# Performance work log

Hardware: AMD Instinct MI355X
Metric: run time of the kernel (lower is better)

The kernel has to match this reference:

```python
import jax, jax.numpy as jnp
import numpy as np

TAU = 2.0        # MultiStepLIFNode tau
ALPHA = 4.0      # sigmoid surrogate-gradient sharpness (spikingjelly default)
BN_EPS = 1e-5

@jax.custom_vjp
def heaviside(x):
    return (x >= 0.0).astype(x.dtype)

def _h_fwd(x):
    return (x >= 0.0).astype(x.dtype), x

def _h_bwd(res, g):
    s = jax.nn.sigmoid(ALPHA * res)
    return (g * ALPHA * s * (1.0 - s),)

heaviside.defvjp(_h_fwd, _h_bwd)

def lif(x_seq, v_threshold=1.0):
    """Multi-step LIF, hard reset to 0, decay_input, detach_reset. x_seq: [T, ...]"""
    def step(v, x):
        v = v + (x - v) / TAU
        spike = heaviside(v - v_threshold)
        v = v * (1.0 - jax.lax.stop_gradient(spike))
        return v, spike
    _, spikes = jax.lax.scan(step, jnp.zeros_like(x_seq[0]), x_seq)
    return spikes

def conv1x1_bn(x, w, gamma, beta, mean, var, bias=None):
    # x: [T,B,C,H,W]; 1x1 conv == channel matmul; BN in eval mode (affine fold)
    y = jnp.einsum('tbchw,oc->tbohw', x, w)
    if bias is not None:
        y = y + bias[None, None, :, None, None]
    inv = gamma / jnp.sqrt(var + BN_EPS)
    return y * inv[None, None, :, None, None] + (beta - mean * inv)[None, None, :, None, None]

def setup_inputs() -> dict:
    key = jax.random.key(0)
    T, B, C, H, W = 4, 16, 512, 32, 32
    ks = jax.random.split(key, 18)
    def w(k):
        return jax.random.normal(k, (C, C), jnp.float32) * (1.0 / np.sqrt(C))
    def vec_n(k):
        return jax.random.normal(k, (C,), jnp.float32) * 0.1
    def vec_p(k):
        return jax.random.uniform(k, (C,), jnp.float32, 0.5, 1.5)
    return {
        'x': jax.random.normal(ks[0], (T, B, C, H, W), jnp.float32),
        'q_w': w(ks[1]), 'q_gamma': vec_p(ks[2]), 'q_beta': vec_n(ks[3]),
        'q_mean': vec_n(ks[4]), 'q_var': vec_p(ks[5]),
        'k_w': w(ks[6]), 'k_gamma': vec_p(ks[7]), 'k_beta': vec_n(ks[8]),
        'k_mean': vec_n(ks[9]), 'k_var': vec_p(ks[10]),
        'proj_w': w(ks[11]), 'proj_b': vec_n(ks[12]), 'proj_gamma': vec_p(ks[13]),
        'proj_beta': vec_n(ks[14]), 'proj_mean': vec_n(ks[15]), 'proj_var': vec_p(ks[16]),
        'num_heads': 8,
    }

def reference(x, q_w, q_gamma, q_beta, q_mean, q_var,
              k_w, k_gamma, k_beta, k_mean, k_var,
              proj_w, proj_b, proj_gamma, proj_beta, proj_mean, proj_var,
              num_heads):
    T, B, C, H, W = x.shape
    hd = C // num_heads
    # Q / K branches: conv1x1 -> BN -> LIF spikes
    q = lif(conv1x1_bn(x, q_w, q_gamma, q_beta, q_mean, q_var))          # [T,B,C,H,W]
    k = lif(conv1x1_bn(x, k_w, k_gamma, k_beta, k_mean, k_var))          # [T,B,C,H,W]
    # sum over head-channel dim (keepdim), spike-gate at threshold 0.5
    q = q.reshape(T, B, num_heads, hd, H, W).sum(axis=3, keepdims=True)  # [T,B,nh,1,H,W]
    attn = lif(q, v_threshold=0.5)                                       # [T,B,nh,1,H,W]
    # elementwise gated attention (broadcast over head channels)
    y = (attn * k.reshape(T, B, num_heads, hd, H, W)).reshape(T, B, C, H, W)
    # projection: conv1x1(+bias) -> BN -> LIF
    y = lif(conv1x1_bn(y, proj_w, proj_gamma, proj_beta, proj_mean, proj_var, bias=proj_b))
    return y
```

## Files before the change

kernel.cpp:

```cpp
#include <hip/hip_runtime.h>
#include <cstdint>
#include <math.h>

#define TT 4
#define BB 16
#define CCH 512
#define HWD 1024
#define NHH 8
#define NW 16
#define MQK 1.5e-4
#define MPROJ 1.0e-4
#define CAPQ 49152
#define CAPP 16384
#define WTSZ 262144

typedef __attribute__((ext_vector_type(4))) float f32x4;
typedef __attribute__((ext_vector_type(8))) short s16x8;
typedef __attribute__((ext_vector_type(4))) uint32_t u32x4;

static __device__ __forceinline__ f32x4 MFMA(s16x8 a, s16x8 b, f32x4 c) {
    return __builtin_amdgcn_mfma_f32_16x16x32_bf16(a, b, c, 0, 0, 0);
}

static __device__ __forceinline__ uint32_t hi_pair(uint32_t u0, uint32_t u1) {
#if __has_builtin(__builtin_amdgcn_perm)
    return __builtin_amdgcn_perm(u1, u0, 0x07060302u);
#else
    return (u1 & 0xFFFF0000u) | (u0 >> 16);
#endif
}
static __device__ __forceinline__ uint32_t lo_pair(uint32_t u0, uint32_t u1) {
#if __has_builtin(__builtin_amdgcn_perm)
    return __builtin_amdgcn_perm(u1, u0, 0x05040100u);
#else
    return ((u1 & 0xFFFFu) << 16) | (u0 & 0xFFFFu);
#endif
}

struct SplitPair { uint32_t h, l; };

static __device__ __forceinline__ SplitPair split_pair(float f0, float f1) {
    const uint32_t u0 = __builtin_bit_cast(uint32_t, f0);
    const uint32_t u1 = __builtin_bit_cast(uint32_t, f1);
    SplitPair r;
    r.h = hi_pair(u0, u1);
    const float r0 = f0 - __builtin_bit_cast(float, u0 & 0xFFFF0000u);
    const float r1 = f1 - __builtin_bit_cast(float, u1 & 0xFFFF0000u);
    r.l = hi_pair(__builtin_bit_cast(uint32_t, r0), __builtin_bit_cast(uint32_t, r1));
    return r;
}

static __device__ __forceinline__ void load_split_frag(const float* p, s16x8& h, s16x8& l) {
    const float4 a = *(const float4*)p;
    const float4 b4 = *(const float4*)(p + 4);
    u32x4 hw_, lw_;
    const SplitPair p0 = split_pair(a.x, a.y);
    const SplitPair p1 = split_pair(a.z, a.w);
    const SplitPair p2 = split_pair(b4.x, b4.y);
    const SplitPair p3 = split_pair(b4.z, b4.w);
    hw_[0] = p0.h; lw_[0] = p0.l;
    hw_[1] = p1.h; lw_[1] = p1.l;
    hw_[2] = p2.h; lw_[2] = p2.l;
    hw_[3] = p3.h; lw_[3] = p3.l;
    h = __builtin_bit_cast(s16x8, hw_);
    l = __builtin_bit_cast(s16x8, lw_);
}

static __device__ __forceinline__ void glds16(const float* g, float* l) {
    __builtin_amdgcn_global_load_lds(
        (const __attribute__((address_space(1))) uint32_t*)g,
        (__attribute__((address_space(3))) uint32_t*)l, 16, 0, 0);
}

static __device__ __forceinline__ void probe_bf16(int lane, int rowD[4], int colD[4],
                                                  int& aRow, int& aKb, int& bCol, int& bKb)
{
    const f32x4 z = {0.f, 0.f, 0.f, 0.f};
    const short lv = (short)(__builtin_bit_cast(uint32_t, (float)lane) >> 16);
    const short one = (short)0x3F80;
    const s16x8 av = {lv, lv, lv, lv, lv, lv, lv, lv};
    const s16x8 ov = {one, one, one, one, one, one, one, one};
    const f32x4 pa = MFMA(av, ov, z);
    const f32x4 pb = MFMA(ov, av, z);
    bool A2 = false, B2 = false;
#pragma unroll
    for (int r = 0; r < 4; ++r) {
        const int va = (int)pa[r];
        if (((va - 48) & 127) == 0) { rowD[r] = (va - 48) >> 7; A2 = true; }
        else                        { rowD[r] = (va - 768) >> 5; }
        const int vb = (int)pb[r];
        if (((vb - 48) & 127) == 0) { colD[r] = (vb - 48) >> 7; B2 = true; }
        else                        { colD[r] = (vb - 768) >> 5; }
    }
    aRow = A2 ? (lane >> 2) : (lane & 15);
    aKb  = A2 ? (lane & 3) * 8 : (lane >> 4) * 8;
    bCol = B2 ? (lane >> 2) : (lane & 15);
    bKb  = B2 ? (lane & 3) * 8 : (lane >> 4) * 8;
}

__global__ void k_zero(unsigned int* ctr) {
    if (threadIdx.x < 2) ctr[threadIdx.x] = 0u;
}

__global__ __launch_bounds__(256) void k_prep(
    const float* __restrict__ qw, const float* __restrict__ kw, const float* __restrict__ pw,
    const float* __restrict__ qg, const float* __restrict__ qbe,
    const float* __restrict__ qm, const float* __restrict__ qva,
    const float* __restrict__ kg, const float* __restrict__ kbe,
    const float* __restrict__ km, const float* __restrict__ kva,
    const float* __restrict__ pg, const float* __restrict__ pbe,
    const float* __restrict__ pm, const float* __restrict__ pva,
    const float* __restrict__ pb,
    unsigned short* __restrict__ wt, double* __restrict__ bnc)
{
    const int bx = blockIdx.x;
    const int mat = bx >> 5, ot = bx & 31;
    const float* W = (mat == 0) ? qw : ((mat == 1) ? kw : pw);
    unsigned short* hi = wt + (size_t)(mat * 2 + 0) * WTSZ;
    unsigned short* lo = wt + (size_t)(mat * 2 + 1) * WTSZ;
#pragma unroll
    for (int it = 0; it < 4; ++it) {
        const int j = it * 256 + threadIdx.x;
        const int ks = j >> 6, sub = j & 63;
        const int kgrp = sub >> 4, row = sub & 15;
        const float* src = W + (size_t)(ot * 16 + row) * CCH + ks * 32 + kgrp * 8;
        s16x8 h, l;
        load_split_frag(src, h, l);
        *(s16x8*)&hi[((size_t)(ot * 16 + ks) * 64 + sub) * 8] = h;
        *(s16x8*)&lo[((size_t)(ot * 16 + ks) * 64 + sub) * 8] = l;
    }
    if (ot == 0) {
        const float* g  = (mat == 0) ? qg  : ((mat == 1) ? kg  : pg);
        const float* be = (mat == 0) ? qbe : ((mat == 1) ? kbe : pbe);
        const float* mn = (mat == 0) ? qm  : ((mat == 1) ? km  : pm);
        const float* va = (mat == 0) ? qva : ((mat == 1) ? kva : pva);
        for (int o = threadIdx.x; o < CCH; o += 256) {
            const double inv = (double)g[o] / sqrt((double)va[o] + 1e-5);
            double add = (double)be[o] - (double)mn[o] * inv;
            if (mat == 2) add = add + (double)pb[o] * inv;
            bnc[(size_t)(mat * CCH + o) * 2]     = inv;
            bnc[(size_t)(mat * CCH + o) * 2 + 1] = add;
        }
    }
}

__global__ __launch_bounds__(256, 4) void k_qk(
    const float* __restrict__ x,
    const unsigned short* __restrict__ wt, const double* __restrict__ bnc,
    uint32_t* __restrict__ qbits, uint32_t* __restrict__ kbits,
    unsigned int* __restrict__ ctr, uint32_t* __restrict__ list)
{
    __shared__ float Xs[2][4096];
    __shared__ uint32_t QB[2][2][TT][32];

    const int tid = threadIdx.x, lane = tid & 63, wid = tid >> 6;
    const int b   = blockIdx.z;
    const int o0  = blockIdx.y * 64, hw0 = blockIdx.x * 32;
    const int worow = (wid >> 1) * 32, whw = (wid & 1) * 16;

    int rowD[4], colD[4], aRow, aKb, bCol, bKb;
    probe_bf16(lane, rowD, colD, aRow, aKb, bCol, bKb);

    const int laneoff = ((aKb >> 3) * 16 + aRow) * 8;
    const int kgrp = bKb >> 3;
    const int roff = (whw + bCol) ^ ((kgrp & 1) << 4);
    const int otg0 = blockIdx.y * 4 + (wid >> 1) * 2;

    uint32_t gOff[4];
#pragma unroll
    for (int it = 0; it < 4; ++it) {
        const int ch = it * 256 + tid;
        const int t = ch >> 8, c = (ch >> 3) & 31, hw4p = ch & 7;
        const int ghw4 = hw4p ^ (((c >> 3) & 1) << 2);
        gOff[it] = (uint32_t)(((t * BB + b) * CCH + c) * HWD + hw0 + ghw4 * 4);
    }

    f32x4 aq[TT][2], ak[TT][2];
#pragma unroll
    for (int t = 0; t < TT; ++t)
#pragma unroll
        for (int ot = 0; ot < 2; ++ot) {
            aq[t][ot] = (f32x4){0.f, 0.f, 0.f, 0.f};
            ak[t][ot] = (f32x4){0.f, 0.f, 0.f, 0.f};
        }

    auto stage = [&](int ks, int buf) {
#pragma unroll
        for (int it = 0; it < 4; ++it)
            glds16(x + (size_t)gOff[it] + (size_t)ks * (32 * HWD),
                   &Xs[buf][(it * 256 + wid * 64) * 4]);
    };

    stage(0, 0);

    int cur = 0;
#pragma unroll 1
    for (int ks = 0; ks < 16; ++ks) {
        __syncthreads();
        if (ks < 15) stage(ks + 1, cur ^ 1);

        const size_t tb0 = ((size_t)(otg0 + 0) * 16 + ks) * 512 + laneoff;
        const size_t tb1 = ((size_t)(otg0 + 1) * 16 + ks) * 512 + laneoff;
        const s16x8 Aqh0 = *(const s16x8*)&wt[0 * WTSZ + tb0];
        const s16x8 Aql0 = *(const s16x8*)&wt[1 * WTSZ + tb0];
        const s16x8 Akh0 = *(const s16x8*)&wt[2 * WTSZ + tb0];
        const s16x8 Akl0 = *(const s16x8*)&wt[3 * WTSZ + tb0];
        const s16x8 Aqh1 = *(const s16x8*)&wt[0 * WTSZ + tb1];
        const s16x8 Aql1 = *(const s16x8*)&wt[1 * WTSZ + tb1];
        const s16x8 Akh1 = *(const s16x8*)&wt[2 * WTSZ + tb1];
        const s16x8 Akl1 = *(const s16x8*)&wt[3 * WTSZ + tb1];

        const float* Bb = Xs[cur];
#pragma unroll
        for (int t = 0; t < TT; ++t) {
            const float* Bp = Bb + (t * 32 + kgrp * 8) * 32 + roff;
            float w[8];
#pragma unroll
            for (int e = 0; e < 8; ++e) w[e] = Bp[e * 32];
            u32x4 bh, bl;
#pragma unroll
            for (int p = 0; p < 4; ++p) {
                const SplitPair sp = split_pair(w[2 * p], w[2 * p + 1]);
                bh[p] = sp.h; bl[p] = sp.l;
            }
            const s16x8 Bh = __builtin_bit_cast(s16x8, bh);
            const s16x8 Bl = __builtin_bit_cast(s16x8, bl);

            aq[t][0] = MFMA(Aqh0, Bh, aq[t][0]);
            aq[t][0] = MFMA(Aqh0, Bl, aq[t][0]);
            aq[t][0] = MFMA(Aql0, Bh, aq[t][0]);
            ak[t][0] = MFMA(Akh0, Bh, ak[t][0]);
            ak[t][0] = MFMA(Akh0, Bl, ak[t][0]);
            ak[t][0] = MFMA(Akl0, Bh, ak[t][0]);
            aq[t][1] = MFMA(Aqh1, Bh, aq[t][1]);
            aq[t][1] = MFMA(Aqh1, Bl, aq[t][1]);
            aq[t][1] = MFMA(Aql1, Bh, aq[t][1]);
            ak[t][1] = MFMA(Akh1, Bh, ak[t][1]);
            ak[t][1] = MFMA(Akh1, Bl, ak[t][1]);
            ak[t][1] = MFMA(Akl1, Bh, ak[t][1]);
        }
        cur ^= 1;
    }

    {
        int dum0, dum1, dum2, dum3;
        probe_bf16(lane, rowD, colD, dum0, dum1, dum2, dum3);
    }
    ((uint32_t*)QB)[tid] = 0u;
    ((uint32_t*)QB)[tid + 256] = 0u;
    __syncthreads();

    auto chains = [&](f32x4 (&acc)[TT][2], int br) {
#pragma unroll
        for (int ot = 0; ot < 2; ++ot)
#pragma unroll
            for (int r = 0; r < 4; ++r) {
                const int orow = worow + ot * 16 + rowD[r];
                const int o = o0 + orow;
                const double inv = bnc[(size_t)(br * CCH + o) * 2];
                const double add = bnc[(size_t)(br * CCH + o) * 2 + 1];
                const uint32_t bit = 1u << (orow & 31);
                const int ow = orow >> 5;
                const int hwq = whw + colD[r];
                double v = 0.0; bool fl = false;
#pragma unroll
                for (int t = 0; t < TT; ++t) {
                    const double y = (double)acc[t][ot][r] * inv + add;
                    v = v + (y - v) * 0.5;
                    if (fabs(v - 1.0) < MQK) fl = true;
                    if (v >= 1.0) { atomicOr(&QB[br][ow][t][hwq], bit); v = 0.0; }
                }
                if (fl) {
                    const unsigned int idx = atomicAdd(ctr, 1u);
                    if (idx < CAPQ)
                        list[idx] = (uint32_t)((br << 23) | (o << 14) | (b << 10) | (hw0 + hwq));
                }
            }
    };
    chains(aq, 0);
    chains(ak, 1);
    __syncthreads();

#pragma unroll
    for (int u = 0; u < 2; ++u) {
        const int idx = tid + u * 256;
        const int br = idx >> 8, ow = (idx >> 7) & 1, t = (idx >> 5) & 3, hwq = idx & 31;
        uint32_t* dst = br ? kbits : qbits;
        dst[((size_t)(t * BB + b) * NW + (o0 >> 5) + ow) * HWD + hw0 + hwq] = QB[br][ow][t][hwq];
    }
}

__global__ __launch_bounds__(256) void k_fix_qk(
    const float* __restrict__ x,
    const float* __restrict__ qw, const float* __restrict__ qg, const float* __restrict__ qbe,
    const float* __restrict__ qm, const float* __restrict__ qva,
    const float* __restrict__ kw, const float* __restrict__ kg, const float* __restrict__ kbe,
    const float* __restrict__ km, const float* __restrict__ kva,
    const unsigned int* __restrict__ ctr, const uint32_t* __restrict__ list,
    uint32_t* __restrict__ qbits, uint32_t* __restrict__ kbits)
{
    const int lane = threadIdx.x & 63;
    const int wg = (blockIdx.x * blockDim.x + threadIdx.x) >> 6;
    const int nw = (gridDim.x * blockDim.x) >> 6;
    unsigned int n = *ctr; if (n > CAPQ) n = CAPQ;

    for (unsigned int i = wg; i < n; i += nw) {
        const uint32_t e = list[i];
        const int br = (e >> 23) & 1, o = (e >> 14) & 511, b = (e >> 10) & 15, hw = e & 1023;
        const float* w = (br ? kw : qw) + (size_t)o * CCH;
        double dots[TT];
#pragma unroll
        for (int t = 0; t < TT; ++t) {
            double s = 0.0;
            for (int c = lane; c < CCH; c += 64)
                s += (double)w[c] * (double)x[((size_t)(t * BB + b) * CCH + c) * HWD + hw];
#pragma unroll
            for (int off = 32; off; off >>= 1) s += __shfl_xor(s, off);
            dots[t] = s;
        }
        if (lane == 0) {
            const float* g  = br ? kg  : qg;
            const float* be = br ? kbe : qbe;
            const float* mn = br ? km  : qm;
            const float* va = br ? kva : qva;
            const double inv = (double)g[o] / sqrt((double)va[o] + 1e-5);
            const double add = (double)be[o] - (double)mn[o] * inv;
            uint32_t* bits = br ? kbits : qbits;
            double v = 0.0;
#pragma unroll
            for (int t = 0; t < TT; ++t) {
                const double y = dots[t] * inv + add;
                v = v + (y - v) * 0.5;
                const size_t wa = ((size_t)(t * BB + b) * NW + (o >> 5)) * HWD + hw;
                const uint32_t bit = 1u << (o & 31);
                if (v >= 1.0) { atomicOr(&bits[wa], bit); v = 0.0; }
                else          { atomicAnd(&bits[wa], ~bit); }
            }
        }
    }
}

__global__ __launch_bounds__(256) void k_attn(
    const uint32_t* __restrict__ qbits, uint8_t* __restrict__ attn)
{
    const int idx = blockIdx.x * 256 + threadIdx.x;
    const int hw = idx & (HWD - 1);
    const int h  = (idx >> 10) & (NHH - 1);
    const int b  = idx >> 13;
    double v = 0.0;
#pragma unroll
    for (int t = 0; t < TT; ++t) {
        const uint32_t w0 = qbits[((size_t)(t * BB + b) * NW + h * 2    ) * HWD + hw];
        const uint32_t w1 = qbits[((size_t)(t * BB + b) * NW + h * 2 + 1) * HWD + hw];
        const double q = (double)(__popc(w0) + __popc(w1));
        v = v + (q - v) * 0.5;
        const uint8_t s = (v >= 0.5) ? (uint8_t)1 : (uint8_t)0;
        attn[((size_t)(t * BB + b) * NHH + h) * HWD + hw] = s;
        if (s) v = 0.0;
    }
}

__global__ __launch_bounds__(256) void k_proj(
    const unsigned short* __restrict__ wt, const double* __restrict__ bnc,
    const uint32_t* __restrict__ kbits, const uint8_t* __restrict__ attn,
    float* __restrict__ out,
    unsigned int* __restrict__ ctr2, uint32_t* __restrict__ list2)
{
    const int tid = threadIdx.x, lane = tid & 63, wid = tid >> 6;
    const int b   = blockIdx.z;
    const int o0  = blockIdx.y * 128, hw0 = blockIdx.x * 32;
    const int worow = (wid >> 1) * 64, whw = (wid & 1) * 16;

    int rowD[4], colD[4], aRow, aKb, bCol, bKb;
    probe_bf16(lane, rowD, colD, aRow, aKb, bCol, bKb);
    const int laneoff = ((aKb >> 3) * 16 + aRow) * 8;
    const int hwB = hw0 + whw + bCol;
    const int otg0 = blockIdx.y * 8 + (wid >> 1) * 4;

    f32x4 acc[TT][4];
#pragma unroll
    for (int t = 0; t < TT; ++t)
#pragma unroll
        for (int ot = 0; ot < 4; ++ot) acc[t][ot] = (f32x4){0.f, 0.f, 0.f, 0.f};

#pragma unroll 1
    for (int ks = 0; ks < 16; ++ks) {
        s16x8 Ah[4], Al[4];
#pragma unroll
        for (int ot = 0; ot < 4; ++ot) {
            const size_t tb = ((size_t)(otg0 + ot) * 16 + ks) * 512 + laneoff;
            Ah[ot] = *(const s16x8*)&wt[4 * WTSZ + tb];
            Al[ot] = *(const s16x8*)&wt[5 * WTSZ + tb];
        }
#pragma unroll
        for (int t = 0; t < TT; ++t) {
            const size_t tb = (size_t)(t * BB + b);
            const uint32_t kv = kbits[(tb * NW + ks) * HWD + hwB];
            const uint32_t av = attn[(tb * NHH + (ks >> 1)) * HWD + hwB];
            const uint32_t mask = av ? kv : 0u;
            const uint32_t byt = (mask >> bKb) & 0xFFu;
            u32x4 bw;
#pragma unroll
            for (int j = 0; j < 4; ++j)
                bw[j] = (((byt >> (2 * j)) & 1u) ? 0x3F80u : 0u)
                      | (((byt >> (2 * j + 1)) & 1u) ? 0x3F800000u : 0u);
            const s16x8 By = __builtin_bit_cast(s16x8, bw);
#pragma unroll
            for (int ot = 0; ot < 4; ++ot) {
                acc[t][ot] = MFMA(Ah[ot], By, acc[t][ot]);
                acc[t][ot] = MFMA(Al[ot], By, acc[t][ot]);
            }
        }
    }

#pragma unroll
    for (int ot = 0; ot < 4; ++ot)
#pragma unroll
        for (int r = 0; r < 4; ++r) {
            const int o = o0 + worow + ot * 16 + rowD[r];
            const int hwD = hw0 + whw + colD[r];
            const double inv = bnc[(size_t)(2 * CCH + o) * 2];
            const double add = bnc[(size_t)(2 * CCH + o) * 2 + 1];
            double v = 0.0; bool fl = false;
#pragma unroll
            for (int t = 0; t < TT; ++t) {
                const double y = (double)acc[t][ot][r] * inv + add;
                v = v + (y - v) * 0.5;
                if (fabs(v - 1.0) < MPROJ) fl = true;
                float s;
                if (v >= 1.0) { s = 1.0f; v = 0.0; } else { s = 0.0f; }
                out[((size_t)(t * BB + b) * CCH + o) * HWD + hwD] = s;
            }
            if (fl) {
                const unsigned int idx = atomicAdd(ctr2, 1u);
                if (idx < CAPP) list2[idx] = (uint32_t)((o << 14) | (b << 10) | hwD);
            }
        }
}

__global__ __launch_bounds__(256) void k_fix_proj(
    const float* __restrict__ pw, const float* __restrict__ pb,
    const float* __restrict__ pg, const float* __restrict__ pbe,
    const float* __restrict__ pm, const float* __restrict__ pva,
    const uint32_t* __restrict__ kbits, const uint8_t* __restrict__ attn,
    const unsigned int* __restrict__ ctr2, const uint32_t* __restrict__ list2,
    float* __restrict__ out)
{
    const int lane = threadIdx.x & 63;
    const int wg = (blockIdx.x * blockDim.x + threadIdx.x) >> 6;
    const int nw = (gridDim.x * blockDim.x) >> 6;
    unsigned int n = *ctr2; if (n > CAPP) n = CAPP;

    for (unsigned int i = wg; i < n; i += nw) {
        const uint32_t e = list2[i];
        const int o = (e >> 14) & 511, b = (e >> 10) & 15, hw = e & 1023;
        const float* w = pw + (size_t)o * CCH;
        double dots[TT];
#pragma unroll
        for (int t = 0; t < TT; ++t) {
            double s = 0.0;
            for (int c = lane; c < CCH; c += 64) {
                const uint32_t kv = kbits[((size_t)(t * BB + b) * NW + (c >> 5)) * HWD + hw];
                const uint32_t av = attn[((size_t)(t * BB + b) * NHH + (c >> 6)) * HWD + hw];
                if (av && ((kv >> (c & 31)) & 1u)) s += (double)w[c];
            }
#pragma unroll
            for (int off = 32; off; off >>= 1) s += __shfl_xor(s, off);
            dots[t] = s;
        }
        if (lane == 0) {
            const double inv = (double)pg[o] / sqrt((double)pva[o] + 1e-5);
            const double add = (double)pbe[o] - (double)pm[o] * inv;
            const double bias = (double)pb[o];
            double v = 0.0;
#pragma unroll
            for (int t = 0; t < TT; ++t) {
                const double y = (dots[t] + bias) * inv + add;
                v = v + (y - v) * 0.5;
                float s;
                if (v >= 1.0) { s = 1.0f; v = 0.0; } else { s = 0.0f; }
                out[((size_t)(t * BB + b) * CCH + o) * HWD + hw] = s;
            }
        }
    }
}

extern "C" void kernel_launch(void* const* d_in, const int* in_sizes, int n_in,
                              void* d_out, int out_size, void* d_ws, size_t ws_size,
                              hipStream_t stream)
{
    (void)in_sizes; (void)n_in; (void)out_size; (void)ws_size;

    const float* x   = (const float*)d_in[0];
    const float* qw  = (const float*)d_in[1];
    const float* qg  = (const float*)d_in[2];
    const float* qbe = (const float*)d_in[3];
    const float* qm  = (const float*)d_in[4];
    const float* qv  = (const float*)d_in[5];
    const float* kw  = (const float*)d_in[6];
    const float* kg  = (const float*)d_in[7];
    const float* kbe = (const float*)d_in[8];
    const float* km  = (const float*)d_in[9];
    const float* kv  = (const float*)d_in[10];
    const float* pw  = (const float*)d_in[11];
    const float* pb  = (const float*)d_in[12];
    const float* pg  = (const float*)d_in[13];
    const float* pbe = (const float*)d_in[14];
    const float* pm  = (const float*)d_in[15];
    const float* pv  = (const float*)d_in[16];

    uint8_t* base = (uint8_t*)d_ws;
    uint32_t* qbits = (uint32_t*)base;
    uint32_t* kbits = (uint32_t*)(base + 4194304);
    uint8_t*  attn  = base + 8388608;
    unsigned int* ctr = (unsigned int*)(base + 8912896);
    uint32_t* qklist  = (uint32_t*)(base + 8913152);
    uint32_t* prlist  = (uint32_t*)(base + 9109760);
    unsigned short* wtiles = (unsigned short*)(base + 9175296);
    double* bnc = (double*)(base + 12321024);
    float* out = (float*)d_out;

    k_zero<<<1, 64, 0, stream>>>(ctr);
    k_prep<<<96, 256, 0, stream>>>(qw, kw, pw, qg, qbe, qm, qv,
                                   kg, kbe, km, kv, pg, pbe, pm, pv, pb,
                                   wtiles, bnc);
    k_qk<<<dim3(HWD / 32, CCH / 64, BB), 256, 0, stream>>>(
        x, wtiles, bnc, qbits, kbits, ctr, qklist);
    k_fix_qk<<<256, 256, 0, stream>>>(x, qw, qg, qbe, qm, qv,
                                      kw, kg, kbe, km, kv, ctr, qklist, qbits, kbits);
    k_attn<<<(BB * NHH * HWD) / 256, 256, 0, stream>>>(qbits, attn);
    k_proj<<<dim3(HWD / 32, CCH / 128, BB), 256, 0, stream>>>(
        wtiles, bnc, kbits, attn, out, ctr + 1, prlist);
    k_fix_proj<<<64, 256, 0, stream>>>(pw, pb, pg, pbe, pm, pv,
                                       kbits, attn, ctr + 1, prlist, out);
}
```

Baseline: 405.6 us.

## Pre-split X tile to bf16 hi/lo once in LDS and widen k_qk to 128 channels

k_qk now loads x into registers, splits each value into bf16 hi/lo parts once, and stores the pre-split halves in padded LDS buffers. Previously every wave re-split the fp32 tile it read from LDS. The block grows to 512 threads covering 128 output channels, so each staged x tile is shared by twice as many output rows. This removes redundant conversion work and halves how often x is re-read per output. The cost is register-staged loads in place of direct global-to-LDS loads, a barrier moved to the end of the loop, and a larger block that may lower occupancy.

New measurement: 402.6 us. Within noise of the previous version (-0.7%).

```diff
diff --git a/kernel.cpp b/kernel.cpp
--- a/kernel.cpp
+++ b/kernel.cpp
@@ -13,10 +13,12 @@
 #define CAPQ 49152
 #define CAPP 16384
 #define WTSZ 262144
+#define XROW 40
 
 typedef __attribute__((ext_vector_type(4))) float f32x4;
 typedef __attribute__((ext_vector_type(8))) short s16x8;
 typedef __attribute__((ext_vector_type(4))) uint32_t u32x4;
+typedef __attribute__((ext_vector_type(2))) uint32_t u32x2;
 
 static __device__ __forceinline__ f32x4 MFMA(s16x8 a, s16x8 b, f32x4 c) {
     return __builtin_amdgcn_mfma_f32_16x16x32_bf16(a, b, c, 0, 0, 0);
@@ -27,13 +29,6 @@
     return __builtin_amdgcn_perm(u1, u0, 0x07060302u);
 #else
     return (u1 & 0xFFFF0000u) | (u0 >> 16);
-#endif
-}
-static __device__ __forceinline__ uint32_t lo_pair(uint32_t u0, uint32_t u1) {
-#if __has_builtin(__builtin_amdgcn_perm)
-    return __builtin_amdgcn_perm(u1, u0, 0x05040100u);
-#else
-    return ((u1 & 0xFFFFu) << 16) | (u0 & 0xFFFFu);
 #endif
 }
 
@@ -66,12 +61,6 @@
     l = __builtin_bit_cast(s16x8, lw_);
 }
 
-static __device__ __forceinline__ void glds16(const float* g, float* l) {
-    __builtin_amdgcn_global_load_lds(
-        (const __attribute__((address_space(1))) uint32_t*)g,
-        (__attribute__((address_space(3))) uint32_t*)l, 16, 0, 0);
-}
-
 static __device__ __forceinline__ void probe_bf16(int lane, int rowD[4], int colD[4],
                                                   int& aRow, int& aKb, int& bCol, int& bKb)
 {
@@ -144,18 +133,19 @@
     }
 }
 
-__global__ __launch_bounds__(256, 4) void k_qk(
+__global__ __launch_bounds__(512, 4) void k_qk(
     const float* __restrict__ x,
     const unsigned short* __restrict__ wt, const double* __restrict__ bnc,
     uint32_t* __restrict__ qbits, uint32_t* __restrict__ kbits,
     unsigned int* __restrict__ ctr, uint32_t* __restrict__ list)
 {
-    __shared__ float Xs[2][4096];
-    __shared__ uint32_t QB[2][2][TT][32];
+    __shared__ unsigned short Xh[2][TT * 32 * XROW];
+    __shared__ unsigned short Xl[2][TT * 32 * XROW];
+    __shared__ uint32_t QB[2][4][TT][32];
 
     const int tid = threadIdx.x, lane = tid & 63, wid = tid >> 6;
     const int b   = blockIdx.z;
-    const int o0  = blockIdx.y * 64, hw0 = blockIdx.x * 32;
+    const int o0  = blockIdx.y * 128, hw0 = blockIdx.x * 32;
     const int worow = (wid >> 1) * 32, whw = (wid & 1) * 16;
 
     int rowD[4], colD[4], aRow, aKb, bCol, bKb;
@@ -163,16 +153,16 @@
 
     const int laneoff = ((aKb >> 3) * 16 + aRow) * 8;
     const int kgrp = bKb >> 3;
-    const int roff = (whw + bCol) ^ ((kgrp & 1) << 4);
-    const int otg0 = blockIdx.y * 4 + (wid >> 1) * 2;
-
-    uint32_t gOff[4];
-#pragma unroll
-    for (int it = 0; it < 4; ++it) {
-        const int ch = it * 256 + tid;
-        const int t = ch >> 8, c = (ch >> 3) & 31, hw4p = ch & 7;
-        const int ghw4 = hw4p ^ (((c >> 3) & 1) << 2);
-        gOff[it] = (uint32_t)(((t * BB + b) * CCH + c) * HWD + hw0 + ghw4 * 4);
+    const int boff = (whw + bCol) * XROW + kgrp * 8;
+    const int otg0 = blockIdx.y * 8 + (wid >> 1) * 2;
+
+    uint32_t gBase[2]; int lOff[2];
+#pragma unroll
+    for (int u = 0; u < 2; ++u) {
+        const int ch = u * 512 + tid;
+        const int shw = ch & 31, cg = (ch >> 5) & 7, t = ch >> 8;
+        gBase[u] = (uint32_t)(((t * BB + b) * CCH + cg * 4) * HWD + hw0 + shw);
+        lOff[u]  = t * 32 * XROW + shw * XROW + cg * 4;
     }
 
     f32x4 aq[TT][2], ak[TT][2];
@@ -184,20 +174,43 @@
             ak[t][ot] = (f32x4){0.f, 0.f, 0.f, 0.f};
         }
 
-    auto stage = [&](int ks, int buf) {
-#pragma unroll
-        for (int it = 0; it < 4; ++it)
-            glds16(x + (size_t)gOff[it] + (size_t)ks * (32 * HWD),
-                   &Xs[buf][(it * 256 + wid * 64) * 4]);
+    float st[2][4];
+    auto loadst = [&](int ks) {
+#pragma unroll
+        for (int u = 0; u < 2; ++u)
+#pragma unroll
+            for (int j = 0; j < 4; ++j)
+                st[u][j] = x[(size_t)gBase[u] + (size_t)(ks * 32 + j) * HWD];
     };
-
-    stage(0, 0);
+    auto stagewrite = [&](int buf) {
+#pragma unroll
+        for (int u = 0; u < 2; ++u) {
+            const uint32_t u0 = __builtin_bit_cast(uint32_t, st[u][0]);
+            const uint32_t u1 = __builtin_bit_cast(uint32_t, st[u][1]);
+            const uint32_t u2 = __builtin_bit_cast(uint32_t, st[u][2]);
+            const uint32_t u3 = __builtin_bit_cast(uint32_t, st[u][3]);
+            u32x2 h, l;
+            h[0] = hi_pair(u0, u1);
+            h[1] = hi_pair(u2, u3);
+            const float r0 = st[u][0] - __builtin_bit_cast(float, u0 & 0xFFFF0000u);
+            const float r1 = st[u][1] - __builtin_bit_cast(float, u1 & 0xFFFF0000u);
+            const float r2 = st[u][2] - __builtin_bit_cast(float, u2 & 0xFFFF0000u);
+            const float r3 = st[u][3] - __builtin_bit_cast(float, u3 & 0xFFFF0000u);
+            l[0] = hi_pair(__builtin_bit_cast(uint32_t, r0), __builtin_bit_cast(uint32_t, r1));
+            l[1] = hi_pair(__builtin_bit_cast(uint32_t, r2), __builtin_bit_cast(uint32_t, r3));
+            *(u32x2*)&Xh[buf][lOff[u]] = h;
+            *(u32x2*)&Xl[buf][lOff[u]] = l;
+        }
+    };
+
+    loadst(0);
+    stagewrite(0);
+    __syncthreads();
 
     int cur = 0;
 #pragma unroll 1
     for (int ks = 0; ks < 16; ++ks) {
-        __syncthreads();
-        if (ks < 15) stage(ks + 1, cur ^ 1);
+        if (ks < 15) loadst(ks + 1);
 
         const size_t tb0 = ((size_t)(otg0 + 0) * 16 + ks) * 512 + laneoff;
         const size_t tb1 = ((size_t)(otg0 + 1) * 16 + ks) * 512 + laneoff;
@@ -210,21 +223,11 @@
         const s16x8 Akh1 = *(const s16x8*)&wt[2 * WTSZ + tb1];
         const s16x8 Akl1 = *(const s16x8*)&wt[3 * WTSZ + tb1];
 
-        const float* Bb = Xs[cur];
 #pragma unroll
         for (int t = 0; t < TT; ++t) {
-            const float* Bp = Bb + (t * 32 + kgrp * 8) * 32 + roff;
-            float w[8];
-#pragma unroll
-            for (int e = 0; e < 8; ++e) w[e] = Bp[e * 32];
-            u32x4 bh, bl;
-#pragma unroll
-            for (int p = 0; p < 4; ++p) {
-                const SplitPair sp = split_pair(w[2 * p], w[2 * p + 1]);
-                bh[p] = sp.h; bl[p] = sp.l;
-            }
-            const s16x8 Bh = __builtin_bit_cast(s16x8, bh);
-            const s16x8 Bl = __builtin_bit_cast(s16x8, bl);
+            const int off = t * 32 * XROW + boff;
+            const s16x8 Bh = *(const s16x8*)&Xh[cur][off];
+            const s16x8 Bl = *(const s16x8*)&Xl[cur][off];
 
             aq[t][0] = MFMA(Aqh0, Bh, aq[t][0]);
             aq[t][0] = MFMA(Aqh0, Bl, aq[t][0]);
@@ -239,15 +242,14 @@
             ak[t][1] = MFMA(Akh1, Bl, ak[t][1]);
             ak[t][1] = MFMA(Akl1, Bh, ak[t][1]);
         }
+
+        if (ks < 15) stagewrite(cur ^ 1);
+        __syncthreads();
         cur ^= 1;
     }
 
-    {
-        int dum0, dum1, dum2, dum3;
-        probe_bf16(lane, rowD, colD, dum0, dum1, dum2, dum3);
-    }
     ((uint32_t*)QB)[tid] = 0u;
-    ((uint32_t*)QB)[tid + 256] = 0u;
+    ((uint32_t*)QB)[tid + 512] = 0u;
     __syncthreads();
 
     auto chains = [&](f32x4 (&acc)[TT][2], int br) {
@@ -283,8 +285,8 @@
 
 #pragma unroll
     for (int u = 0; u < 2; ++u) {
-        const int idx = tid + u * 256;
-        const int br = idx >> 8, ow = (idx >> 7) & 1, t = (idx >> 5) & 3, hwq = idx & 31;
+        const int idx = tid + u * 512;
+        const int br = idx >> 9, ow = (idx >> 7) & 3, t = (idx >> 5) & 3, hwq = idx & 31;
         uint32_t* dst = br ? kbits : qbits;
         dst[((size_t)(t * BB + b) * NW + (o0 >> 5) + ow) * HWD + hw0 + hwq] = QB[br][ow][t][hwq];
     }
@@ -524,7 +526,7 @@
     k_prep<<<96, 256, 0, stream>>>(qw, kw, pw, qg, qbe, qm, qv,
                                    kg, kbe, km, kv, pg, pbe, pm, pv, pb,
                                    wtiles, bnc);
-    k_qk<<<dim3(HWD / 32, CCH / 64, BB), 256, 0, stream>>>(
+    k_qk<<<dim3(HWD / 32, CCH / 128, BB), 512, 0, stream>>>(
         x, wtiles, bnc, qbits, kbits, ctr, qklist);
     k_fix_qk<<<256, 256, 0, stream>>>(x, qw, qg, qbe, qm, qv,
                                       kw, kg, kbe, km, kv, ctr, qklist, qbits, kbits);
```

## Pre-split X tiles to bf16 hi/lo in LDS via register staging

Applied to the files above, without the earlier changes.

Replaces the direct global-to-LDS fp32 copies of the X tile with register-staged loads that split each value into bf16 hi/lo pairs once, before writing them to separate LDS arrays. In the MFMA loop each wave reads packed pairs directly, so the split work is no longer repeated by each of the four waves reading the same data. The prefetch moves into registers and overlaps with the MFMAs. In exchange, register pressure rises (launch bounds lowered from 4 to 3 blocks per CU) and the async LDS load path is dropped. A leftover redundant probe call and unused helpers are also removed.

Result: no change. 413.5 us (+2.0%).

```diff
diff --git a/kernel.cpp b/kernel.cpp
--- a/kernel.cpp
+++ b/kernel.cpp
@@ -27,13 +27,6 @@
     return __builtin_amdgcn_perm(u1, u0, 0x07060302u);
 #else
     return (u1 & 0xFFFF0000u) | (u0 >> 16);
-#endif
-}
-static __device__ __forceinline__ uint32_t lo_pair(uint32_t u0, uint32_t u1) {
-#if __has_builtin(__builtin_amdgcn_perm)
-    return __builtin_amdgcn_perm(u1, u0, 0x05040100u);
-#else
-    return ((u1 & 0xFFFFu) << 16) | (u0 & 0xFFFFu);
 #endif
 }
 
@@ -66,12 +59,6 @@
     l = __builtin_bit_cast(s16x8, lw_);
 }
 
-static __device__ __forceinline__ void glds16(const float* g, float* l) {
-    __builtin_amdgcn_global_load_lds(
-        (const __attribute__((address_space(1))) uint32_t*)g,
-        (__attribute__((address_space(3))) uint32_t*)l, 16, 0, 0);
-}
-
 static __device__ __forceinline__ void probe_bf16(int lane, int rowD[4], int colD[4],
                                                   int& aRow, int& aKb, int& bCol, int& bKb)
 {
@@ -144,13 +131,14 @@
     }
 }
 
-__global__ __launch_bounds__(256, 4) void k_qk(
+__global__ __launch_bounds__(256, 3) void k_qk(
     const float* __restrict__ x,
     const unsigned short* __restrict__ wt, const double* __restrict__ bnc,
     uint32_t* __restrict__ qbits, uint32_t* __restrict__ kbits,
     unsigned int* __restrict__ ctr, uint32_t* __restrict__ list)
 {
-    __shared__ float Xs[2][4096];
+    __shared__ uint32_t Xh[2][2048];
+    __shared__ uint32_t Xl[2][2048];
     __shared__ uint32_t QB[2][2][TT][32];
 
     const int tid = threadIdx.x, lane = tid & 63, wid = tid >> 6;
@@ -163,16 +151,18 @@
 
     const int laneoff = ((aKb >> 3) * 16 + aRow) * 8;
     const int kgrp = bKb >> 3;
-    const int roff = (whw + bCol) ^ ((kgrp & 1) << 4);
+    const int roff  = (whw + bCol) ^ ((kgrp & 1) << 4);
+    const int rbase = kgrp * 128 + roff;
     const int otg0 = blockIdx.y * 4 + (wid >> 1) * 2;
 
-    uint32_t gOff[4];
-#pragma unroll
-    for (int it = 0; it < 4; ++it) {
-        const int ch = it * 256 + tid;
-        const int t = ch >> 8, c = (ch >> 3) & 31, hw4p = ch & 7;
-        const int ghw4 = hw4p ^ (((c >> 3) & 1) << 2);
-        gOff[it] = (uint32_t)(((t * BB + b) * CCH + c) * HWD + hw0 + ghw4 * 4);
+    uint32_t gOff[4]; int wOff[4];
+#pragma unroll
+    for (int u = 0; u < 4; ++u) {
+        const int ch = u * 256 + tid;
+        const int t = ch >> 8, cg = (ch >> 5) & 7, shw = ch & 31;
+        gOff[u] = (uint32_t)(((t * BB + b) * CCH + cg * 4) * HWD + hw0 + shw);
+        const int hwp = shw ^ (((cg >> 1) & 1) << 4);
+        wOff[u] = t * 512 + (cg * 2) * 32 + hwp;
     }
 
     f32x4 aq[TT][2], ak[TT][2];
@@ -184,20 +174,34 @@
             ak[t][ot] = (f32x4){0.f, 0.f, 0.f, 0.f};
         }
 
-    auto stage = [&](int ks, int buf) {
-#pragma unroll
-        for (int it = 0; it < 4; ++it)
-            glds16(x + (size_t)gOff[it] + (size_t)ks * (32 * HWD),
-                   &Xs[buf][(it * 256 + wid * 64) * 4]);
+    float st[4][4];
+    auto loadst = [&](int ks) {
+#pragma unroll
+        for (int u = 0; u < 4; ++u)
+#pragma unroll
+            for (int j = 0; j < 4; ++j)
+                st[u][j] = x[(size_t)gOff[u] + (size_t)(ks * 32 + j) * HWD];
     };
-
-    stage(0, 0);
+    auto stagewrite = [&](int buf) {
+#pragma unroll
+        for (int u = 0; u < 4; ++u) {
+            const SplitPair s01 = split_pair(st[u][0], st[u][1]);
+            const SplitPair s23 = split_pair(st[u][2], st[u][3]);
+            Xh[buf][wOff[u]]      = s01.h;
+            Xh[buf][wOff[u] + 32] = s23.h;
+            Xl[buf][wOff[u]]      = s01.l;
+            Xl[buf][wOff[u] + 32] = s23.l;
+        }
+    };
+
+    loadst(0);
+    stagewrite(0);
+    __syncthreads();
 
     int cur = 0;
 #pragma unroll 1
     for (int ks = 0; ks < 16; ++ks) {
-        __syncthreads();
-        if (ks < 15) stage(ks + 1, cur ^ 1);
+        if (ks < 15) loadst(ks + 1);
 
         const size_t tb0 = ((size_t)(otg0 + 0) * 16 + ks) * 512 + laneoff;
         const size_t tb1 = ((size_t)(otg0 + 1) * 16 + ks) * 512 + laneoff;
@@ -210,18 +214,14 @@
         const s16x8 Akh1 = *(const s16x8*)&wt[2 * WTSZ + tb1];
         const s16x8 Akl1 = *(const s16x8*)&wt[3 * WTSZ + tb1];
 
-        const float* Bb = Xs[cur];
 #pragma unroll
         for (int t = 0; t < TT; ++t) {
-            const float* Bp = Bb + (t * 32 + kgrp * 8) * 32 + roff;
-            float w[8];
-#pragma unroll
-            for (int e = 0; e < 8; ++e) w[e] = Bp[e * 32];
+            const int ro = t * 512 + rbase;
             u32x4 bh, bl;
 #pragma unroll
             for (int p = 0; p < 4; ++p) {
-                const SplitPair sp = split_pair(w[2 * p], w[2 * p + 1]);
-                bh[p] = sp.h; bl[p] = sp.l;
+                bh[p] = Xh[cur][ro + p * 32];
+                bl[p] = Xl[cur][ro + p * 32];
             }
             const s16x8 Bh = __builtin_bit_cast(s16x8, bh);
             const s16x8 Bl = __builtin_bit_cast(s16x8, bl);
@@ -239,13 +239,12 @@
             ak[t][1] = MFMA(Akh1, Bl, ak[t][1]);
             ak[t][1] = MFMA(Akl1, Bh, ak[t][1]);
         }
+
+        if (ks < 15) stagewrite(cur ^ 1);
+        __syncthreads();
         cur ^= 1;
     }
 
-    {
-        int dum0, dum1, dum2, dum3;
-        probe_bf16(lane, rowD, colD, dum0, dum1, dum2, dum3);
-    }
     ((uint32_t*)QB)[tid] = 0u;
     ((uint32_t*)QB)[tid + 256] = 0u;
     __syncthreads();
```

## Double-buffer projection weights in LDS and prefetch spike bits in k_proj

Applied to the files above, without the earlier changes.

k_proj now stages each k-step's hi/lo bf16 weight tiles into a double-buffered shared-memory array with async global-to-LDS copies, so the block loads them once and shares them instead of every wave reading global memory. The kbits and attn words for the next k-step are prefetched into registers while the current step's MFMAs run. A __syncthreads per iteration and a launch-bounds occupancy hint of 3 are added. The extra barriers and register pressure could offset the gain from overlapping loads.

After: 392.3 us, median of 2. 3.3% less time.

```diff
diff --git a/kernel.cpp b/kernel.cpp
--- a/kernel.cpp
+++ b/kernel.cpp
@@ -27,13 +27,6 @@
     return __builtin_amdgcn_perm(u1, u0, 0x07060302u);
 #else
     return (u1 & 0xFFFF0000u) | (u0 >> 16);
-#endif
-}
-static __device__ __forceinline__ uint32_t lo_pair(uint32_t u0, uint32_t u1) {
-#if __has_builtin(__builtin_amdgcn_perm)
-    return __builtin_amdgcn_perm(u1, u0, 0x05040100u);
-#else
-    return ((u1 & 0xFFFFu) << 16) | (u0 & 0xFFFFu);
 #endif
 }
 
@@ -360,12 +353,14 @@
     }
 }
 
-__global__ __launch_bounds__(256) void k_proj(
+__global__ __launch_bounds__(256, 3) void k_proj(
     const unsigned short* __restrict__ wt, const double* __restrict__ bnc,
     const uint32_t* __restrict__ kbits, const uint8_t* __restrict__ attn,
     float* __restrict__ out,
     unsigned int* __restrict__ ctr2, uint32_t* __restrict__ list2)
 {
+    __shared__ __align__(16) unsigned short Aw[2][2][8][512];
+
     const int tid = threadIdx.x, lane = tid & 63, wid = tid >> 6;
     const int b   = blockIdx.z;
     const int o0  = blockIdx.y * 128, hw0 = blockIdx.x * 32;
@@ -375,7 +370,7 @@
     probe_bf16(lane, rowD, colD, aRow, aKb, bCol, bKb);
     const int laneoff = ((aKb >> 3) * 16 + aRow) * 8;
     const int hwB = hw0 + whw + bCol;
-    const int otg0 = blockIdx.y * 8 + (wid >> 1) * 4;
+    const int otl0 = (wid >> 1) * 4;
 
     f32x4 acc[TT][4];
 #pragma unroll
@@ -383,21 +378,45 @@
 #pragma unroll
         for (int ot = 0; ot < 4; ++ot) acc[t][ot] = (f32x4){0.f, 0.f, 0.f, 0.f};
 
+    auto stageA = [&](int ks, int buf) {
+#pragma unroll
+        for (int i = 0; i < 4; ++i) {
+            const int ch = wid * 4 + i;
+            const int plane = ch >> 3, otl = ch & 7;
+            const unsigned short* src = wt + (size_t)(4 + plane) * WTSZ
+                + ((size_t)(blockIdx.y * 8 + otl) * 16 + ks) * 512 + (size_t)lane * 8;
+            glds16((const float*)src, (float*)&Aw[buf][plane][otl][0]);
+        }
+    };
+
+    uint32_t kvc[TT], avc[TT], kvn[TT], avn[TT];
+    auto loadB = [&](int ks, uint32_t kv[TT], uint32_t av[TT]) {
+#pragma unroll
+        for (int t = 0; t < TT; ++t) {
+            const size_t tb = (size_t)(t * BB + b);
+            kv[t] = kbits[(tb * NW + ks) * HWD + hwB];
+            av[t] = attn[(tb * NHH + (ks >> 1)) * HWD + hwB];
+        }
+    };
+
+    stageA(0, 0);
+    loadB(0, kvc, avc);
+    __syncthreads();
+
+    int cur = 0;
 #pragma unroll 1
     for (int ks = 0; ks < 16; ++ks) {
+        if (ks < 15) { stageA(ks + 1, cur ^ 1); loadB(ks + 1, kvn, avn); }
+
         s16x8 Ah[4], Al[4];
 #pragma unroll
         for (int ot = 0; ot < 4; ++ot) {
-            const size_t tb = ((size_t)(otg0 + ot) * 16 + ks) * 512 + laneoff;
-            Ah[ot] = *(const s16x8*)&wt[4 * WTSZ + tb];
-            Al[ot] = *(const s16x8*)&wt[5 * WTSZ + tb];
+            Ah[ot] = *(const s16x8*)&Aw[cur][0][otl0 + ot][laneoff];
+            Al[ot] = *(const s16x8*)&Aw[cur][1][otl0 + ot][laneoff];
         }
 #pragma unroll
         for (int t = 0; t < TT; ++t) {
-            const size_t tb = (size_t)(t * BB + b);
-            const uint32_t kv = kbits[(tb * NW + ks) * HWD + hwB];
-            const uint32_t av = attn[(tb * NHH + (ks >> 1)) * HWD + hwB];
-            const uint32_t mask = av ? kv : 0u;
+            const uint32_t mask = avc[t] ? kvc[t] : 0u;
             const uint32_t byt = (mask >> bKb) & 0xFFu;
             u32x4 bw;
 #pragma unroll
@@ -411,6 +430,13 @@
                 acc[t][ot] = MFMA(Al[ot], By, acc[t][ot]);
             }
         }
+
+        if (ks < 15) {
+#pragma unroll
+            for (int t = 0; t < TT; ++t) { kvc[t] = kvn[t]; avc[t] = avn[t]; }
+        }
+        __syncthreads();
+        cur ^= 1;
     }
 
 #pragma unroll
```
